# Kernel tuning notes

Measured on AMD Instinct MI355X. Metric: run time of the kernel, lower is better.

The kernel has to match this reference:

```python
import jax, jax.numpy as jnp
import numpy as np

N = 10000      # nodes
E = 160000     # edges (before self-loops)
IN = 256
NEG_SLOPE = 0.2  # PyG GATConv default


def gat_layer(x, src, dst, W, a_src, a_dst, bias, heads, concat, n):
    # x: [n, in_dim]; W: [in_dim, heads*C]; a_src/a_dst: [heads, C]
    C = W.shape[1] // heads
    h = (x @ W).reshape(n, heads, C)                      # [n,H,C]
    es = jnp.einsum('nhc,hc->nh', h, a_src)               # [n,H]
    ed = jnp.einsum('nhc,hc->nh', h, a_dst)               # [n,H]
    e = jax.nn.leaky_relu(es[src] + ed[dst], NEG_SLOPE)   # [E,H]
    # segment softmax over destination node (every node has a self-loop)
    emax = jax.ops.segment_max(e, dst, num_segments=n)    # [n,H]
    al = jnp.exp(e - emax[dst])                           # [E,H]
    den = jax.ops.segment_sum(al, dst, num_segments=n)    # [n,H]
    al = al / den[dst]
    out = jax.ops.segment_sum(h[src] * al[:, :, None], dst, num_segments=n)  # [n,H,C]
    out = out.reshape(n, heads * C) if concat else out.mean(axis=1)
    return out + bias


def setup_inputs() -> dict:
    key = jax.random.key(0)
    ks = jax.random.split(key, 16)
    s = 0.05
    p = lambda k, shp: jax.random.normal(k, shp, dtype=jnp.float32) * s
    return {
        'x': jax.random.normal(ks[0], (N, IN), dtype=jnp.float32),
        'edge_index': jax.random.randint(ks[1], (2, E), 0, N, dtype=jnp.int64),
        'proj_w': p(ks[2], (IN, 512)), 'proj_b': jnp.zeros((512,), jnp.float32),
        'w1': p(ks[3], (512, 4 * 512)),  'as1': p(ks[4], (4, 512)), 'ad1': p(ks[5], (4, 512)),  'b1': jnp.zeros((2048,), jnp.float32),
        'w2': p(ks[6], (2048, 4 * 512)), 'as2': p(ks[7], (4, 512)), 'ad2': p(ks[8], (4, 512)),  'b2': jnp.zeros((2048,), jnp.float32),
        'w3': p(ks[9], (2048, 2 * 512)), 'as3': p(ks[10], (2, 512)), 'ad3': p(ks[11], (2, 512)), 'b3': jnp.zeros((512,), jnp.float32),
    }


def reference(x, edge_index, proj_w, proj_b, w1, as1, ad1, b1,
              w2, as2, ad2, b2, w3, as3, ad3, b3):
    n = x.shape[0]
    loops = jnp.arange(n, dtype=edge_index.dtype)
    src = jnp.concatenate([edge_index[0], loops])   # PyG add_self_loops=True
    dst = jnp.concatenate([edge_index[1], loops])
    h = x @ proj_w + proj_b                         # dropout is identity in eval
    h = gat_layer(h, src, dst, w1, as1, ad1, b1, 4, True, n)
    h = jax.nn.elu(h)
    h = gat_layer(h, src, dst, w2, as2, ad2, b2, 4, True, n)
    h = jax.nn.elu(h)
    h = gat_layer(h, src, dst, w3, as3, ad3, b3, 2, False, n)
    return h
```

## Files before the change

### kernel.cpp

```cpp
#include <hip/hip_runtime.h>
#include <hip/hip_bf16.h>
#include <math.h>

#define CDIV(a,b) (((a)+(b)-1)/(b))

typedef __bf16  bf16x8 __attribute__((ext_vector_type(8)));
typedef float   f32x4  __attribute__((ext_vector_type(4)));
typedef unsigned short u16x8 __attribute__((ext_vector_type(8)));
typedef unsigned short u16x4 __attribute__((ext_vector_type(4)));

__device__ __forceinline__ float bf2f(unsigned short u) {
    union { unsigned int i; float f; } x; x.i = ((unsigned int)u) << 16; return x.f;
}
__device__ __forceinline__ unsigned short f2bf(float f) {
    union { float f; unsigned int i; } x; x.f = f;
    unsigned int r = x.i + 0x7fff + ((x.i >> 16) & 1);
    return (unsigned short)(r >> 16);
}

__global__ void hist_kernel(const int* __restrict__ ei, int* __restrict__ deg,
                            int E, int Et) {
    int e = blockIdx.x * blockDim.x + threadIdx.x;
    if (e >= Et) return;
    int d = (e < E) ? ei[E + e] : (e - E);
    atomicAdd(&deg[d], 1);
}

__global__ void scan_kernel(const int* __restrict__ deg, int* __restrict__ off, int n) {
    __shared__ int wsum[16];
    __shared__ int carry_s;
    int t = threadIdx.x, lane = t & 63, wv = t >> 6;
    if (t == 0) carry_s = 0;
    __syncthreads();
    for (int base = 0; base < n; base += 1024) {
        int v = (base + t < n) ? deg[base + t] : 0;
        int x = v;
#pragma unroll
        for (int o = 1; o < 64; o <<= 1) {
            int y = __shfl_up(x, o);
            if (lane >= o) x += y;
        }
        if (lane == 63) wsum[wv] = x;
        __syncthreads();
        if (wv == 0 && lane < 16) {
            int s = wsum[lane];
#pragma unroll
            for (int o = 1; o < 16; o <<= 1) {
                int y = __shfl_up(s, o);
                if (lane >= o) s += y;
            }
            wsum[lane] = s;
        }
        __syncthreads();
        int wprev = (wv == 0) ? 0 : wsum[wv - 1];
        int incl = carry_s + wprev + x;
        if (base + t < n) off[base + t] = incl - v;
        __syncthreads();
        if (t == 1023) carry_s = incl;
        __syncthreads();
    }
    if (t == 0) off[n] = carry_s;
}

__global__ void scatter_kernel(const int* __restrict__ ei, const int* __restrict__ off,
                               int* __restrict__ cur, int* __restrict__ csr,
                               int E, int Et) {
    int e = blockIdx.x * blockDim.x + threadIdx.x;
    if (e >= Et) return;
    int s, d;
    if (e < E) { s = ei[e]; d = ei[E + e]; } else { s = e - E; d = s; }
    int pos = off[d] + atomicAdd(&cur[d], 1);
    csr[pos] = s;
}

__global__ void prep_t_kernel(const float* __restrict__ wa, __hip_bfloat16* __restrict__ wta,
                              const float* __restrict__ wb, __hip_bfloat16* __restrict__ wtb,
                              const float* __restrict__ wc, __hip_bfloat16* __restrict__ wtc,
                              int t0, int t1, int t2) {
    __shared__ float tile[32][33];
    int bid = blockIdx.x;
    const float* w; __hip_bfloat16* wt; int K, N, r;
    if (bid < t0)      { w = wa; wt = wta; K = 512;  N = 2048; r = bid; }
    else if (bid < t1) { w = wb; wt = wtb; K = 2048; N = 2048; r = bid - t0; }
    else               { w = wc; wt = wtc; K = 2048; N = 1024; r = bid - t1; }
    (void)t2;
    int kt = K >> 5;
    int kb = (r % kt) * 32, nb = (r / kt) * 32;
    int tx = threadIdx.x & 31, ty = threadIdx.x >> 5;
    for (int i = ty; i < 32; i += 8)
        tile[i][tx] = w[(size_t)(kb + i) * N + nb + tx];
    __syncthreads();
    for (int i = ty; i < 32; i += 8)
        wt[(size_t)(nb + i) * K + kb + tx] = __float2bfloat16(tile[tx][i]);
}

__global__ void cvt2_kernel(const float* __restrict__ a, __hip_bfloat16* __restrict__ ao,
                            int na4,
                            const float* __restrict__ b, __hip_bfloat16* __restrict__ bo,
                            int nb4) {
    int i = blockIdx.x * blockDim.x + threadIdx.x;
    const float* src; __hip_bfloat16* dst; int idx;
    if (i < na4) { src = a; dst = ao; idx = i * 4; }
    else if (i < na4 + nb4) { src = b; dst = bo; idx = (i - na4) * 4; }
    else return;
    float4 v = *(const float4*)(src + idx);
    dst[idx + 0] = __float2bfloat16(v.x);
    dst[idx + 1] = __float2bfloat16(v.y);
    dst[idx + 2] = __float2bfloat16(v.z);
    dst[idx + 3] = __float2bfloat16(v.w);
}

__global__ void beff_kernel(const float* __restrict__ pb, const float* __restrict__ w1,
                            float* __restrict__ beff, int N) {
    int j  = blockIdx.x * 256 + threadIdx.x;
    int k0 = blockIdx.y * 64;
    float s = 0.f;
#pragma unroll
    for (int k = 0; k < 64; k++)
        s = fmaf(pb[k0 + k], w1[(size_t)(k0 + k) * N + j], s);
    atomicAdd(&beff[j], s);
}

__device__ __forceinline__ void gload16(void* lds, const void* g) {
    __builtin_amdgcn_global_load_lds(
        (const __attribute__((address_space(1))) void*)g,
        (__attribute__((address_space(3))) void*)lds, 16, 0, 0);
}

__global__ __launch_bounds__(256) void gemm_bf16_kernel(
    const __hip_bfloat16* __restrict__ A,
    const __hip_bfloat16* __restrict__ BT,
    const float* __restrict__ bias,
    __hip_bfloat16* __restrict__ Cb,
    int M, int N, int K, int MB, int NB, int XT)
{
    __shared__ __align__(16) __hip_bfloat16 As[128 * 32];
    __shared__ __align__(16) __hip_bfloat16 Bs[128 * 32];

    const int bid  = blockIdx.x;
    const int xcd  = bid & 7;
    const int slot = bid >> 3;
    const int x_sub = slot / NB;
    const int yb    = slot - x_sub * NB;
    const int xb    = xcd * XT + x_sub;
    if (xb >= MB) return;

    const int tid = threadIdx.x;
    const int m0 = xb * 128, n0 = yb * 128;
    const int w = tid >> 6, l = tid & 63;
    const int wm = (w & 1) * 64, wn = (w >> 1) * 64;
    const int lm = l & 15, lq = l >> 4;

    f32x4 acc[4][4] = {};

    const int arow = tid >> 2;
    const int acol = (tid & 3) * 8;
    const __hip_bfloat16* Ag = A  + (size_t)(m0 + arow) * K + acol;
    const __hip_bfloat16* Bg = BT + (size_t)(n0 + arow) * K + acol;
    char* AsW = (char*)As + (w << 10);
    char* BsW = (char*)Bs + (w << 10);

    for (int k0 = 0; k0 < K; k0 += 32) {
        gload16(AsW,        Ag + k0);
        gload16(AsW + 4096, Ag + (size_t)64 * K + k0);
        gload16(BsW,        Bg + k0);
        gload16(BsW + 4096, Bg + (size_t)64 * K + k0);
        __syncthreads();
        bf16x8 af[4], bfr[4];
#pragma unroll
        for (int i = 0; i < 4; i++)
            af[i] = *(const bf16x8*)(As + (wm + i * 16 + lm) * 32 + lq * 8);
#pragma unroll
        for (int j = 0; j < 4; j++)
            bfr[j] = *(const bf16x8*)(Bs + (wn + j * 16 + lm) * 32 + lq * 8);
#pragma unroll
        for (int i = 0; i < 4; i++)
#pragma unroll
            for (int j = 0; j < 4; j++)
                acc[i][j] = __builtin_amdgcn_mfma_f32_16x16x32_bf16(
                    af[i], bfr[j], acc[i][j], 0, 0, 0);
        __syncthreads();
    }

#pragma unroll
    for (int i = 0; i < 4; i++) {
        int rb = m0 + wm + i * 16 + lq * 4;
#pragma unroll
        for (int r = 0; r < 4; r++) {
            int row = rb + r;
            if (row >= M) continue;
#pragma unroll
            for (int j = 0; j < 4; j++) {
                int col = n0 + wn + j * 16 + lm;
                float v = acc[i][j][r];
                if (bias) v += bias[col];
                Cb[(size_t)row * N + col] = __float2bfloat16(v);
            }
        }
    }
}

__global__ void esed_kernel(const __hip_bfloat16* __restrict__ h,
                            const float* __restrict__ a_src,
                            const float* __restrict__ a_dst,
                            float* __restrict__ es, float* __restrict__ ed, int H) {
    int nidx = blockIdx.x;
    int t = threadIdx.x;
    int head = t >> 6, lane = t & 63;
    const unsigned short* hp =
        (const unsigned short*)h + (size_t)nidx * H * 512 + head * 512 + lane * 8;
    const float* sp = a_src + head * 512 + lane * 8;
    const float* dp = a_dst + head * 512 + lane * 8;
    u16x8 hv = *(const u16x8*)hp;
    float4 s0 = *(const float4*)sp, s1 = *(const float4*)(sp + 4);
    float4 d0 = *(const float4*)dp, d1 = *(const float4*)(dp + 4);
    float hf[8];
#pragma unroll
    for (int k = 0; k < 8; k++) hf[k] = bf2f(hv[k]);
    float s = hf[0]*s0.x + hf[1]*s0.y + hf[2]*s0.z + hf[3]*s0.w
            + hf[4]*s1.x + hf[5]*s1.y + hf[6]*s1.z + hf[7]*s1.w;
    float d = hf[0]*d0.x + hf[1]*d0.y + hf[2]*d0.z + hf[3]*d0.w
            + hf[4]*d1.x + hf[5]*d1.y + hf[6]*d1.z + hf[7]*d1.w;
    for (int o = 32; o; o >>= 1) { s += __shfl_down(s, o); d += __shfl_down(d, o); }
    if (lane == 0) { es[nidx * H + head] = s; ed[nidx * H + head] = d; }
}

template<int H, int VEC, bool MEAN>
__global__ __launch_bounds__(256) void agg_kernel(
    const __hip_bfloat16* __restrict__ h, const float* __restrict__ es,
    const float* __restrict__ ed, const int* __restrict__ csr,
    const int* __restrict__ off, const float* __restrict__ bias,
    float* __restrict__ outF, __hip_bfloat16* __restrict__ outB, int do_elu)
{
    constexpr int HS = H * 512;
    __shared__ float red[MEAN ? 1024 : 1];
    int d = blockIdx.x, t = threadIdx.x;
    int c0 = t * VEC;
    int head = c0 >> 9;
    float edd = ed[d * H + head];
    int beg = off[d], end = off[d + 1];
    float acc[VEC];
#pragma unroll
    for (int k = 0; k < VEC; k++) acc[k] = 0.f;
    float den = 0.f;
    const unsigned short* hb = (const unsigned short*)h;

    int i = beg;
    for (; i + 3 < end; i += 4) {
        int   s[4];
        float wgt[4];
#pragma unroll
        for (int u = 0; u < 4; u++) {
            s[u] = csr[i + u];
            float e = es[s[u] * H + head] + edd;
            e = (e > 0.f) ? e : 0.2f * e;
            wgt[u] = __expf(e);
        }
        if constexpr (VEC == 8) {
            u16x8 v[4];
#pragma unroll
            for (int u = 0; u < 4; u++)
                v[u] = *(const u16x8*)(hb + (size_t)s[u] * HS + c0);
#pragma unroll
            for (int u = 0; u < 4; u++) {
                den += wgt[u];
#pragma unroll
                for (int k = 0; k < 8; k++) acc[k] = fmaf(wgt[u], bf2f(v[u][k]), acc[k]);
            }
        } else {
            u16x4 v[4];
#pragma unroll
            for (int u = 0; u < 4; u++)
                v[u] = *(const u16x4*)(hb + (size_t)s[u] * HS + c0);
#pragma unroll
            for (int u = 0; u < 4; u++) {
                den += wgt[u];
#pragma unroll
                for (int k = 0; k < VEC; k++) acc[k] = fmaf(wgt[u], bf2f(v[u][k]), acc[k]);
            }
        }
    }
    for (; i < end; i++) {
        int s0 = csr[i];
        float e0 = es[s0 * H + head] + edd;
        e0 = (e0 > 0.f) ? e0 : 0.2f * e0;
        float w0 = __expf(e0);
        den += w0;
        const unsigned short* hp0 = hb + (size_t)s0 * HS + c0;
        if constexpr (VEC == 8) {
            u16x8 v0 = *(const u16x8*)hp0;
#pragma unroll
            for (int k = 0; k < 8; k++) acc[k] = fmaf(w0, bf2f(v0[k]), acc[k]);
        } else {
            u16x4 v0 = *(const u16x4*)hp0;
#pragma unroll
            for (int k = 0; k < VEC; k++) acc[k] = fmaf(w0, bf2f(v0[k]), acc[k]);
        }
    }

    float inv = 1.f / den;
    if constexpr (!MEAN) {
        u16x8 ov;
#pragma unroll
        for (int k = 0; k < VEC; k++) {
            float v = acc[k] * inv + bias[c0 + k];
            if (do_elu) v = (v > 0.f) ? v : expm1f(v);
            ov[k] = f2bf(v);
        }
        *(u16x8*)((unsigned short*)outB + (size_t)d * HS + c0) = ov;
    } else {
#pragma unroll
        for (int k = 0; k < VEC; k++) red[c0 + k] = acc[k] * inv;
        __syncthreads();
        if (t < 128) {
#pragma unroll
            for (int k = 0; k < 4; k++) {
                int c = t * 4 + k;
                outF[(size_t)d * 512 + c] = 0.5f * (red[c] + red[c + 512]) + bias[c];
            }
        }
    }
}

extern "C" void kernel_launch(void* const* d_in, const int* in_sizes, int n_in,
                              void* d_out, int out_size, void* d_ws, size_t ws_size,
                              hipStream_t stream) {
    const float* x      = (const float*)d_in[0];
    const int*   ei     = (const int*)  d_in[1];
    const float* proj_w = (const float*)d_in[2];
    const float* proj_b = (const float*)d_in[3];
    const float* w1  = (const float*)d_in[4];
    const float* as1 = (const float*)d_in[5];
    const float* ad1 = (const float*)d_in[6];
    const float* b1  = (const float*)d_in[7];
    const float* w2  = (const float*)d_in[8];
    const float* as2 = (const float*)d_in[9];
    const float* ad2 = (const float*)d_in[10];
    const float* b2  = (const float*)d_in[11];
    const float* w3  = (const float*)d_in[12];
    const float* as3 = (const float*)d_in[13];
    const float* ad3 = (const float*)d_in[14];
    const float* b3  = (const float*)d_in[15];

    const int n    = in_sizes[0] / 256;
    const int E    = in_sizes[1] / 2;
    const int Et   = E + n;
    const int MB   = CDIV(n, 128);
    const int Mpad = MB * 128;
    const int XT   = CDIV(MB, 8);

    char* p = (char*)d_ws;
    auto carve = [&](size_t bytes) {
        void* r = (void*)p;
        p += (bytes + 255) & ~(size_t)255;
        return r;
    };
    __hip_bfloat16* h_bf    = (__hip_bfloat16*)carve((size_t)Mpad * 2048 * sizeof(__hip_bfloat16));
    __hip_bfloat16* act_bf  = (__hip_bfloat16*)carve((size_t)Mpad * 2048 * sizeof(__hip_bfloat16));
    __hip_bfloat16* x_bf    = (__hip_bfloat16*)carve((size_t)Mpad * 256 * sizeof(__hip_bfloat16));
    __hip_bfloat16* pw_bf   = (__hip_bfloat16*)carve((size_t)256 * 512 * sizeof(__hip_bfloat16));
    __hip_bfloat16* w1t     = (__hip_bfloat16*)carve((size_t)2048 * 512 * sizeof(__hip_bfloat16));
    __hip_bfloat16* w2t     = (__hip_bfloat16*)carve((size_t)2048 * 2048 * sizeof(__hip_bfloat16));
    __hip_bfloat16* w3t     = (__hip_bfloat16*)carve((size_t)1024 * 2048 * sizeof(__hip_bfloat16));
    __hip_bfloat16* w_efft  = (__hip_bfloat16*)carve((size_t)2048 * 256 * sizeof(__hip_bfloat16));
    float* b_eff = (float*)carve((size_t)2048 * sizeof(float));
    float* es  = (float*)carve((size_t)n * 4 * sizeof(float));
    float* ed  = (float*)carve((size_t)n * 4 * sizeof(float));
    int* deg = (int*)carve((size_t)2 * n * sizeof(int));
    int* cur = deg + n;
    int* off = (int*)carve((size_t)(n + 1) * sizeof(int));
    int* csr = (int*)carve((size_t)Et * sizeof(int));
    (void)ws_size; (void)n_in;

    hipMemsetAsync(deg, 0, 2 * n * sizeof(int), stream);
    hipMemsetAsync(b_eff, 0, 2048 * sizeof(float), stream);
    hist_kernel<<<CDIV(Et, 256), 256, 0, stream>>>(ei, deg, E, Et);
    scan_kernel<<<1, 1024, 0, stream>>>(deg, off, n);
    scatter_kernel<<<CDIV(Et, 256), 256, 0, stream>>>(ei, off, cur, csr, E, Et);

    const int t0 = (512 / 32) * (2048 / 32);
    const int t1 = t0 + (2048 / 32) * (2048 / 32);
    const int t2 = t1 + (2048 / 32) * (1024 / 32);
    prep_t_kernel<<<t2, 256, 0, stream>>>(w1, w1t, w2, w2t, w3, w3t, t0, t1, t2);
    const int na4 = 256 * 512 / 4, nb4 = n * 256 / 4;
    cvt2_kernel<<<CDIV(na4 + nb4, 256), 256, 0, stream>>>(proj_w, pw_bf, na4, x, x_bf, nb4);

    gemm_bf16_kernel<<<8 * 2 * 2, 256, 0, stream>>>(
        w1t, pw_bf, nullptr, w_efft, 2048, 256, 512, 16, 2, 2);
    beff_kernel<<<dim3(2048 / 256, 512 / 64), 256, 0, stream>>>(proj_b, w1, b_eff, 2048);

    auto gemm_grid = [&](int NB) { return 8 * XT * NB; };

    gemm_bf16_kernel<<<gemm_grid(16), 256, 0, stream>>>(
        x_bf, w_efft, b_eff, h_bf, n, 2048, 256, MB, 16, XT);
    esed_kernel<<<n, 4 * 64, 0, stream>>>(h_bf, as1, ad1, es, ed, 4);
    agg_kernel<4, 8, false><<<n, 256, 0, stream>>>(h_bf, es, ed, csr, off, b1,
                                                   nullptr, act_bf, 1);

    gemm_bf16_kernel<<<gemm_grid(16), 256, 0, stream>>>(
        act_bf, w2t, nullptr, h_bf, n, 2048, 2048, MB, 16, XT);
    esed_kernel<<<n, 4 * 64, 0, stream>>>(h_bf, as2, ad2, es, ed, 4);
    agg_kernel<4, 8, false><<<n, 256, 0, stream>>>(h_bf, es, ed, csr, off, b2,
                                                   nullptr, act_bf, 1);

    gemm_bf16_kernel<<<gemm_grid(8), 256, 0, stream>>>(
        act_bf, w3t, nullptr, h_bf, n, 1024, 2048, MB, 8, XT);
    esed_kernel<<<n, 2 * 64, 0, stream>>>(h_bf, as3, ad3, es, ed, 2);
    agg_kernel<2, 4, true><<<n, 256, 0, stream>>>(h_bf, es, ed, csr, off, b3,
                                                  (float*)d_out, nullptr, 0);
}
```

Before: 667.0 us.

## Aggregate raw 256-dim inputs before layer-1 projection and fuse ELU into GEMM

Layer 1 is linear in x, so attention logits are computed directly from x using precomputed vectors W_eff·a plus bias constants. Neighbour aggregation then runs on the 256-wide input for each of the 4 heads, and the GEMM projects the aggregated per-head features, with bias and ELU fused into its epilogue. This replaces gathering 2048-wide rows per edge with 256-wide rows and removes the separate esed pass for layer 1. In exchange it adds small precompute kernels, and a strided A operand per head block is handled through the new lda and head-offset GEMM arguments.

New measurement: 635.3 us. 1.05x faster.

```diff
diff --git a/kernel.cpp b/kernel.cpp
--- a/kernel.cpp
+++ b/kernel.cpp
@@ -121,6 +121,108 @@
     atomicAdd(&beff[j], s);
 }
 
+__global__ void va_kernel(const __hip_bfloat16* __restrict__ w_efft,
+                          const float* __restrict__ b_eff,
+                          const float* __restrict__ as1, const float* __restrict__ ad1,
+                          const float* __restrict__ b1,
+                          float* __restrict__ va, float* __restrict__ cvec,
+                          float* __restrict__ b1s) {
+    int j = blockIdx.x, t = threadIdx.x;
+    if (j == 8) {
+        for (int i = t; i < 2048; i += 256) b1s[i] = b_eff[i] + b1[i];
+        return;
+    }
+    int h = j & 3;
+    const float* a = ((j < 4) ? as1 : ad1) + h * 512;
+    __shared__ float aLDS[512];
+    __shared__ float red[256];
+    for (int c = t; c < 512; c += 256) aLDS[c] = a[c];
+    __syncthreads();
+    float acc = 0.f;
+    const unsigned short* wb = (const unsigned short*)w_efft + (size_t)h * 512 * 256 + t;
+    for (int c = 0; c < 512; c++)
+        acc = fmaf(aLDS[c], bf2f(wb[(size_t)c * 256]), acc);
+    va[j * 256 + t] = acc;
+    float cp = b_eff[h * 512 + t] * aLDS[t] + b_eff[h * 512 + 256 + t] * aLDS[256 + t];
+    red[t] = cp;
+    __syncthreads();
+    for (int s = 128; s > 0; s >>= 1) {
+        if (t < s) red[t] += red[t + s];
+        __syncthreads();
+    }
+    if (t == 0) cvec[j] = red[0];
+}
+
+__global__ void es1_kernel(const __hip_bfloat16* __restrict__ x_bf,
+                           const float* __restrict__ va, const float* __restrict__ cvec,
+                           float* __restrict__ es, float* __restrict__ ed) {
+    int node = blockIdx.x, l = threadIdx.x;
+    u16x4 xv = *(const u16x4*)((const unsigned short*)x_bf + (size_t)node * 256 + l * 4);
+    float xf[4];
+#pragma unroll
+    for (int k = 0; k < 4; k++) xf[k] = bf2f(xv[k]);
+    float dot[8];
+#pragma unroll
+    for (int j = 0; j < 8; j++) {
+        float4 v = *(const float4*)(va + j * 256 + l * 4);
+        dot[j] = xf[0] * v.x + xf[1] * v.y + xf[2] * v.z + xf[3] * v.w;
+    }
+#pragma unroll
+    for (int j = 0; j < 8; j++)
+        for (int o = 32; o; o >>= 1) dot[j] += __shfl_down(dot[j], o);
+    if (l == 0) {
+#pragma unroll
+        for (int h = 0; h < 4; h++) {
+            es[node * 4 + h] = dot[h] + cvec[h];
+            ed[node * 4 + h] = dot[4 + h] + cvec[4 + h];
+        }
+    }
+}
+
+__global__ __launch_bounds__(256) void agg1x_kernel(
+    const __hip_bfloat16* __restrict__ x_bf, const float* __restrict__ es,
+    const float* __restrict__ ed, const int* __restrict__ csr,
+    const int* __restrict__ off, __hip_bfloat16* __restrict__ z)
+{
+    __shared__ float alds[64][4];
+    __shared__ int   slds[64];
+    int d = blockIdx.x, t = threadIdx.x;
+    int beg = off[d], end = off[d + 1];
+    float acc[4] = {0.f, 0.f, 0.f, 0.f}, den[4] = {0.f, 0.f, 0.f, 0.f};
+    float edd[4];
+#pragma unroll
+    for (int h = 0; h < 4; h++) edd[h] = ed[d * 4 + h];
+    const unsigned short* xb = (const unsigned short*)x_bf;
+
+    for (int cb = beg; cb < end; cb += 64) {
+        int cl = end - cb; if (cl > 64) cl = 64;
+        int i = t >> 2, h = t & 3;
+        if (i < cl) {
+            int s = csr[cb + i];
+            if (h == 0) slds[i] = s;
+            float e = es[s * 4 + h] + edd[h];
+            e = (e > 0.f) ? e : 0.2f * e;
+            alds[i][h] = __expf(e);
+        }
+        __syncthreads();
+        for (int ii = 0; ii < cl; ii++) {
+            int s = slds[ii];
+            float xv = bf2f(xb[(size_t)s * 256 + t]);
+#pragma unroll
+            for (int hh = 0; hh < 4; hh++) {
+                float a = alds[ii][hh];
+                den[hh] += a;
+                acc[hh] = fmaf(a, xv, acc[hh]);
+            }
+        }
+        __syncthreads();
+    }
+    unsigned short* zb = (unsigned short*)z + (size_t)d * 1024;
+#pragma unroll
+    for (int h = 0; h < 4; h++)
+        zb[h * 256 + t] = f2bf(acc[h] / den[h]);
+}
+
 __device__ __forceinline__ void gload16(void* lds, const void* g) {
     __builtin_amdgcn_global_load_lds(
         (const __attribute__((address_space(1))) void*)g,
@@ -132,7 +234,8 @@
     const __hip_bfloat16* __restrict__ BT,
     const float* __restrict__ bias,
     __hip_bfloat16* __restrict__ Cb,
-    int M, int N, int K, int MB, int NB, int XT)
+    int M, int N, int K, int lda, int hko, int do_elu,
+    int MB, int NB, int XT)
 {
     __shared__ __align__(16) __hip_bfloat16 As[128 * 32];
     __shared__ __align__(16) __hip_bfloat16 Bs[128 * 32];
@@ -155,14 +258,14 @@
 
     const int arow = tid >> 2;
     const int acol = (tid & 3) * 8;
-    const __hip_bfloat16* Ag = A  + (size_t)(m0 + arow) * K + acol;
+    const __hip_bfloat16* Ag = A + (size_t)(m0 + arow) * lda + acol + (n0 >> 9) * hko;
     const __hip_bfloat16* Bg = BT + (size_t)(n0 + arow) * K + acol;
     char* AsW = (char*)As + (w << 10);
     char* BsW = (char*)Bs + (w << 10);
 
     for (int k0 = 0; k0 < K; k0 += 32) {
         gload16(AsW,        Ag + k0);
-        gload16(AsW + 4096, Ag + (size_t)64 * K + k0);
+        gload16(AsW + 4096, Ag + (size_t)64 * lda + k0);
         gload16(BsW,        Bg + k0);
         gload16(BsW + 4096, Bg + (size_t)64 * K + k0);
         __syncthreads();
@@ -194,6 +297,7 @@
                 int col = n0 + wn + j * 16 + lm;
                 float v = acc[i][j][r];
                 if (bias) v += bias[col];
+                if (do_elu) v = (v > 0.f) ? v : expm1f(v);
                 Cb[(size_t)row * N + col] = __float2bfloat16(v);
             }
         }
@@ -364,12 +468,16 @@
     __hip_bfloat16* w3t     = (__hip_bfloat16*)carve((size_t)1024 * 2048 * sizeof(__hip_bfloat16));
     __hip_bfloat16* w_efft  = (__hip_bfloat16*)carve((size_t)2048 * 256 * sizeof(__hip_bfloat16));
     float* b_eff = (float*)carve((size_t)2048 * sizeof(float));
+    float* b1s   = (float*)carve((size_t)2048 * sizeof(float));
+    float* va    = (float*)carve((size_t)8 * 256 * sizeof(float));
+    float* cvec  = (float*)carve((size_t)8 * sizeof(float));
     float* es  = (float*)carve((size_t)n * 4 * sizeof(float));
     float* ed  = (float*)carve((size_t)n * 4 * sizeof(float));
     int* deg = (int*)carve((size_t)2 * n * sizeof(int));
     int* cur = deg + n;
     int* off = (int*)carve((size_t)(n + 1) * sizeof(int));
     int* csr = (int*)carve((size_t)Et * sizeof(int));
+    __hip_bfloat16* z_bf = h_bf;
     (void)ws_size; (void)n_in;
 
     hipMemsetAsync(deg, 0, 2 * n * sizeof(int), stream);
@@ -386,25 +494,26 @@
     cvt2_kernel<<<CDIV(na4 + nb4, 256), 256, 0, stream>>>(proj_w, pw_bf, na4, x, x_bf, nb4);
 
     gemm_bf16_kernel<<<8 * 2 * 2, 256, 0, stream>>>(
-        w1t, pw_bf, nullptr, w_efft, 2048, 256, 512, 16, 2, 2);
+        w1t, pw_bf, nullptr, w_efft, 2048, 256, 512, 512, 0, 0, 16, 2, 2);
     beff_kernel<<<dim3(2048 / 256, 512 / 64), 256, 0, stream>>>(proj_b, w1, b_eff, 2048);
 
+    va_kernel<<<9, 256, 0, stream>>>(w_efft, b_eff, as1, ad1, b1, va, cvec, b1s);
+
     auto gemm_grid = [&](int NB) { return 8 * XT * NB; };
 
+    es1_kernel<<<n, 64, 0, stream>>>(x_bf, va, cvec, es, ed);
+    agg1x_kernel<<<n, 256, 0, stream>>>(x_bf, es, ed, csr, off, z_bf);
     gemm_bf16_kernel<<<gemm_grid(16), 256, 0, stream>>>(
-        x_bf, w_efft, b_eff, h_bf, n, 2048, 256, MB, 16, XT);
-    esed_kernel<<<n, 4 * 64, 0, stream>>>(h_bf, as1, ad1, es, ed, 4);
-    agg_kernel<4, 8, false><<<n, 256, 0, stream>>>(h_bf, es, ed, csr, off, b1,
-                                                   nullptr, act_bf, 1);
+        z_bf, w_efft, b1s, act_bf, n, 2048, 256, 1024, 256, 1, MB, 16, XT);
 
     gemm_bf16_kernel<<<gemm_grid(16), 256, 0, stream>>>(
-        act_bf, w2t, nullptr, h_bf, n, 2048, 2048, MB, 16, XT);
+        act_bf, w2t, nullptr, h_bf, n, 2048, 2048, 2048, 0, 0, MB, 16, XT);
     esed_kernel<<<n, 4 * 64, 0, stream>>>(h_bf, as2, ad2, es, ed, 4);
     agg_kernel<4, 8, false><<<n, 256, 0, stream>>>(h_bf, es, ed, csr, off, b2,
                                                    nullptr, act_bf, 1);
 
     gemm_bf16_kernel<<<gemm_grid(8), 256, 0, stream>>>(
-        act_bf, w3t, nullptr, h_bf, n, 1024, 2048, MB, 8, XT);
+        act_bf, w3t, nullptr, h_bf, n, 1024, 2048, 2048, 0, 0, MB, 8, XT);
     esed_kernel<<<n, 2 * 64, 0, stream>>>(h_bf, as3, ad3, es, ed, 2);
     agg_kernel<2, 4, true><<<n, 256, 0, stream>>>(h_bf, es, ed, csr, off, b3,
                                                   (float*)d_out, nullptr, 0);
```
